# Performance work log

Hardware: AMD Instinct MI355X
Metric: run time of the kernel (lower is better)

Reference implementation:

```python
import jax, jax.numpy as jnp
import numpy as np
import math

DIM = 2048
N_HEADS = 16
N_KV_HEADS = 8
HEAD_DIM = DIM // N_HEADS  # 128
N_REP = N_HEADS // N_KV_HEADS  # 2
SEQ = 2048
BATCH = 1
HIDDEN = 5632  # round_up(int(2*(4*2048)/3), 256)
NORM_EPS = 1e-5
LN_EPS = 1e-5  # torch.nn.LayerNorm default
ROPE_THETA = 10000.0


def rmsnorm(x, w, eps=NORM_EPS):
    x32 = x.astype(jnp.float32)
    n = x32 * jax.lax.rsqrt(jnp.mean(x32 * x32, axis=-1, keepdims=True) + eps)
    return n.astype(x.dtype) * w


def layernorm(x, w, b, eps=LN_EPS):
    mu = jnp.mean(x, axis=-1, keepdims=True)
    var = jnp.mean((x - mu) ** 2, axis=-1, keepdims=True)
    return (x - mu) * jax.lax.rsqrt(var + eps) * w + b


def apply_rope(x, cos, sin):
    # x: [B,S,H,hd]; cos/sin: [S, hd//2] -> complex multiply on (even, odd) pairs
    xr = x.reshape(*x.shape[:-1], HEAD_DIM // 2, 2)
    x0, x1 = xr[..., 0], xr[..., 1]
    c = cos[None, :, None, :]
    s = sin[None, :, None, :]
    o0 = x0 * c - x1 * s
    o1 = x0 * s + x1 * c
    return jnp.stack([o0, o1], axis=-1).reshape(x.shape)


def setup_inputs() -> dict:
    key = jax.random.key(0)
    ks = jax.random.split(key, 10)
    scale = 0.02
    x = jax.random.normal(ks[0], (BATCH, SEQ, DIM), jnp.float32)
    # RoPE tables
    inv_freq = 1.0 / (ROPE_THETA ** (jnp.arange(0, HEAD_DIM, 2, dtype=jnp.float32) / HEAD_DIM))
    ang = jnp.arange(SEQ, dtype=jnp.float32)[:, None] * inv_freq[None, :]  # [S, hd//2]
    freqs_cos = jnp.cos(ang)
    freqs_sin = jnp.sin(ang)
    # causal additive mask
    mask = jnp.where(jnp.tril(jnp.ones((SEQ, SEQ), bool)), 0.0, -1e9).astype(jnp.float32)
    wqkv = jax.random.normal(ks[1], ((N_HEADS + 2 * N_KV_HEADS) * HEAD_DIM, DIM), jnp.float32) * scale
    wo = jax.random.normal(ks[2], (DIM, N_HEADS * HEAD_DIM), jnp.float32) * scale
    qn_w = jnp.ones((HEAD_DIM,), jnp.float32)
    qn_b = jnp.zeros((HEAD_DIM,), jnp.float32)
    kn_w = jnp.ones((HEAD_DIM,), jnp.float32)
    kn_b = jnp.zeros((HEAD_DIM,), jnp.float32)
    attn_norm_w = jnp.ones((DIM,), jnp.float32)
    ffn_norm_w = jnp.ones((DIM,), jnp.float32)
    w13 = jax.random.normal(ks[3], (2 * HIDDEN, DIM), jnp.float32) * scale
    w2 = jax.random.normal(ks[4], (DIM, HIDDEN), jnp.float32) * scale
    return dict(x=x, freqs_cos=freqs_cos, freqs_sin=freqs_sin, mask=mask,
                wqkv=wqkv, wo=wo, qn_w=qn_w, qn_b=qn_b, kn_w=kn_w, kn_b=kn_b,
                attn_norm_w=attn_norm_w, ffn_norm_w=ffn_norm_w, w13=w13, w2=w2)


def reference(x, freqs_cos, freqs_sin, mask, wqkv, wo, qn_w, qn_b, kn_w, kn_b,
              attn_norm_w, ffn_norm_w, w13, w2):
    B, S, _ = x.shape
    # ---- attention sublayer (pre-norm) ----
    h = rmsnorm(x, attn_norm_w)
    qkv = h @ wqkv.T  # [B,S,(H+2KV)*hd]
    q_sz = N_HEADS * HEAD_DIM
    kv_sz = N_KV_HEADS * HEAD_DIM
    q = qkv[..., :q_sz].reshape(B, S, N_HEADS, HEAD_DIM)
    k = qkv[..., q_sz:q_sz + kv_sz].reshape(B, S, N_KV_HEADS, HEAD_DIM)
    v = qkv[..., q_sz + kv_sz:].reshape(B, S, N_KV_HEADS, HEAD_DIM)
    # QK-LayerNorm (per head_dim)
    q = layernorm(q, qn_w, qn_b)
    k = layernorm(k, kn_w, kn_b)
    # RoPE
    q = apply_rope(q, freqs_cos, freqs_sin)
    k = apply_rope(k, freqs_cos, freqs_sin)
    # GQA: repeat kv heads (interleaved like torch repeat_interleave on head dim)
    k = jnp.repeat(k, N_REP, axis=2)
    v = jnp.repeat(v, N_REP, axis=2)
    # scores with fp32 softmax
    scores = jnp.einsum('bqhd,bkhd->bhqk', q, k) / math.sqrt(HEAD_DIM)
    scores = scores + mask[None, None, :, :]
    p = jax.nn.softmax(scores.astype(jnp.float32), axis=-1).astype(q.dtype)
    o = jnp.einsum('bhqk,bkhd->bqhd', p, v).reshape(B, S, N_HEADS * HEAD_DIM)
    attn_out = o @ wo.T
    h = x + attn_out
    # ---- SwiGLU FFN sublayer ----
    g = rmsnorm(h, ffn_norm_w)
    x13 = g @ w13.T
    x1, x3 = x13[..., :HIDDEN], x13[..., HIDDEN:]
    out = h + (jax.nn.silu(x1) * x3) @ w2.T
    return out
```

## Files before the change

### kernel.cpp

```cpp
#include <hip/hip_runtime.h>
#include <math.h>

#define DIM 2048
#define SEQ 2048
#define NH 16
#define NKV 8
#define HD 128
#define HIDDEN 5632
#define QKV_N 4096
#define FF_N 11264

typedef __attribute__((ext_vector_type(8))) short s16x8;
typedef __attribute__((ext_vector_type(4))) float f32x4;

#define GPTR(p) ((const __attribute__((address_space(1))) void*)(p))
#define LPTR(p) ((__attribute__((address_space(3))) void*)(p))

#define CFENCE() __asm__ __volatile__("" ::: "memory")
#define BAR() do { CFENCE(); __builtin_amdgcn_s_barrier(); CFENCE(); } while (0)

__device__ __forceinline__ unsigned short f2bf(float f) {
    union { float f; unsigned u; } v; v.f = f;
    unsigned r = v.u + 0x7fff + ((v.u >> 16) & 1);
    return (unsigned short)(r >> 16);
}
__device__ __forceinline__ float bf2f(unsigned short s) {
    union { unsigned u; float f; } v; v.u = ((unsigned)s) << 16;
    return v.f;
}

__global__ __launch_bounds__(256) void k_cvt(const float* __restrict__ src,
                                             unsigned short* __restrict__ dst, int n4) {
    int i = blockIdx.x * 256 + threadIdx.x;
    if (i < n4) {
        float4 v = ((const float4*)src)[i];
        ushort4 o;
        o.x = f2bf(v.x); o.y = f2bf(v.y); o.z = f2bf(v.z); o.w = f2bf(v.w);
        ((ushort4*)dst)[i] = o;
    }
}

__global__ __launch_bounds__(256) void k_rmsnorm(const float* __restrict__ x,
                                                 const float* __restrict__ w,
                                                 unsigned short* __restrict__ out) {
    int row = blockIdx.x;
    int tid = threadIdx.x, wv = tid >> 6, lane = tid & 63;
    const float* xr = x + (size_t)row * DIM;
    float4 a = ((const float4*)xr)[tid * 2];
    float4 b = ((const float4*)xr)[tid * 2 + 1];
    float ss = a.x*a.x + a.y*a.y + a.z*a.z + a.w*a.w
             + b.x*b.x + b.y*b.y + b.z*b.z + b.w*b.w;
    for (int off = 32; off >= 1; off >>= 1) ss += __shfl_xor(ss, off);
    __shared__ float red[4];
    if (lane == 0) red[wv] = ss;
    __syncthreads();
    float tot = red[0] + red[1] + red[2] + red[3];
    float rs = rsqrtf(tot * (1.0f / DIM) + 1e-5f);
    float4 wa = ((const float4*)w)[tid * 2];
    float4 wb = ((const float4*)w)[tid * 2 + 1];
    ushort4 o0, o1;
    o0.x = f2bf(a.x * rs * wa.x); o0.y = f2bf(a.y * rs * wa.y);
    o0.z = f2bf(a.z * rs * wa.z); o0.w = f2bf(a.w * rs * wa.w);
    o1.x = f2bf(b.x * rs * wb.x); o1.y = f2bf(b.y * rs * wb.y);
    o1.z = f2bf(b.z * rs * wb.z); o1.w = f2bf(b.w * rs * wb.w);
    ushort4* orow = (ushort4*)(out + (size_t)row * DIM);
    orow[tid * 2] = o0; orow[tid * 2 + 1] = o1;
}

template<int ID>
__global__ __launch_bounds__(512, 2) void k_gemm256(
    const unsigned short* __restrict__ A, const unsigned short* __restrict__ B,
    int M, int N, int K, int Kslice,
    float* __restrict__ Cf, unsigned short* __restrict__ Cb,
    const float* __restrict__ add, int flags) {
    __shared__ __align__(16) unsigned short As[2][16384];
    __shared__ __align__(16) unsigned short Bs[2][16384];
    int tid = threadIdx.x;
    int wv = tid >> 6, lane = tid & 63, quad = lane >> 4, l15 = lane & 15;
    int wr = wv >> 2, wc = wv & 3;
    int rowBase = blockIdx.y * 256;
    int colBase = blockIdx.x * 256;
    int kb = blockIdx.z * Kslice;
    int NT = Kslice >> 6;

    f32x4 acc[8][4] = {};

    int srow = lane >> 3;
    int schunk = lane & 7;

    auto stage = [&](const unsigned short* Mat, int matBase,
                     unsigned short (*Ls)[16384], int t, int h, int b) {
#pragma unroll
        for (int j = 0; j < 2; j++) {
            int r0 = h * 128 + (j * 8 + wv) * 8;
            int row = r0 + srow;
            int kchunk = schunk ^ (row & 7);
            const unsigned short* g = Mat + (size_t)(matBase + row) * K
                                      + (kb + t * 64 + kchunk * 8);
            __builtin_amdgcn_global_load_lds(GPTR(g), LPTR(&Ls[b][r0 * 64]), 16, 0, 0);
        }
    };
    auto LDA = [&](int b_, int mt, int ks) -> s16x8 {
        int row = wr * 128 + mt * 16 + l15;
        return *(const s16x8*)&As[b_][row * 64 + ((((ks * 4 + quad)) ^ (row & 7)) << 3)];
    };
    auto LDB = [&](int b_, int nt, int ks) -> s16x8 {
        int row = wc * 64 + nt * 16 + l15;
        return *(const s16x8*)&Bs[b_][row * 64 + ((((ks * 4 + quad)) ^ (row & 7)) << 3)];
    };

    stage(B, colBase, Bs, 0, 0, 0); stage(B, colBase, Bs, 0, 1, 0);
    stage(A, rowBase, As, 0, 0, 0); stage(A, rowBase, As, 0, 1, 0);
    if (NT > 1) {
        stage(B, colBase, Bs, 1, 0, 1); stage(B, colBase, Bs, 1, 1, 1);
        stage(A, rowBase, As, 1, 0, 1); stage(A, rowBase, As, 1, 1, 1);
        asm volatile("s_waitcnt vmcnt(8)" ::: "memory");
    } else {
        asm volatile("s_waitcnt vmcnt(0)" ::: "memory");
    }
    BAR();

    for (int T = 0; T < NT; T++) {
        const int b = T & 1;
        s16x8 a0[8], a1[8], b0[4], b1[4];
#pragma unroll
        for (int mt = 0; mt < 8; mt++) a0[mt] = LDA(b, mt, 0);
#pragma unroll
        for (int nt = 0; nt < 4; nt++) b0[nt] = LDB(b, nt, 0);
        BAR();
        asm volatile("s_waitcnt lgkmcnt(0)" ::: "memory");
        __builtin_amdgcn_s_setprio(1);
#pragma unroll
        for (int mt = 0; mt < 8; mt++) {
            acc[mt][0] = __builtin_amdgcn_mfma_f32_16x16x32_bf16(a0[mt], b0[0], acc[mt][0], 0, 0, 0);
            acc[mt][1] = __builtin_amdgcn_mfma_f32_16x16x32_bf16(a0[mt], b0[1], acc[mt][1], 0, 0, 0);
        }
        __builtin_amdgcn_s_setprio(0);
        BAR();
#pragma unroll
        for (int nt = 0; nt < 4; nt++) b1[nt] = LDB(b, nt, 1);
        BAR();
        asm volatile("s_waitcnt lgkmcnt(0)" ::: "memory");
        __builtin_amdgcn_s_setprio(1);
#pragma unroll
        for (int mt = 0; mt < 8; mt++) {
            acc[mt][2] = __builtin_amdgcn_mfma_f32_16x16x32_bf16(a0[mt], b0[2], acc[mt][2], 0, 0, 0);
            acc[mt][3] = __builtin_amdgcn_mfma_f32_16x16x32_bf16(a0[mt], b0[3], acc[mt][3], 0, 0, 0);
        }
        __builtin_amdgcn_s_setprio(0);
        BAR();
#pragma unroll
        for (int mt = 0; mt < 8; mt++) a1[mt] = LDA(b, mt, 1);
        if (T + 2 < NT) { stage(B, colBase, Bs, T + 2, 0, b); stage(B, colBase, Bs, T + 2, 1, b); }
        BAR();
        asm volatile("s_waitcnt lgkmcnt(0)" ::: "memory");
        __builtin_amdgcn_s_setprio(1);
#pragma unroll
        for (int mt = 0; mt < 8; mt++) {
            acc[mt][0] = __builtin_amdgcn_mfma_f32_16x16x32_bf16(a1[mt], b1[0], acc[mt][0], 0, 0, 0);
            acc[mt][1] = __builtin_amdgcn_mfma_f32_16x16x32_bf16(a1[mt], b1[1], acc[mt][1], 0, 0, 0);
        }
        __builtin_amdgcn_s_setprio(0);
        BAR();
        if (T + 2 < NT) { stage(A, rowBase, As, T + 2, 0, b); stage(A, rowBase, As, T + 2, 1, b); }
        BAR();
        __builtin_amdgcn_s_setprio(1);
#pragma unroll
        for (int mt = 0; mt < 8; mt++) {
            acc[mt][2] = __builtin_amdgcn_mfma_f32_16x16x32_bf16(a1[mt], b1[2], acc[mt][2], 0, 0, 0);
            acc[mt][3] = __builtin_amdgcn_mfma_f32_16x16x32_bf16(a1[mt], b1[3], acc[mt][3], 0, 0, 0);
        }
        __builtin_amdgcn_s_setprio(0);
        if (T + 2 < NT) asm volatile("s_waitcnt vmcnt(8)" ::: "memory");
        else            asm volatile("s_waitcnt vmcnt(0)" ::: "memory");
        BAR();
    }

    float* Cfz = Cf ? Cf + (size_t)blockIdx.z * M * N : nullptr;
#pragma unroll
    for (int mt = 0; mt < 8; mt++)
#pragma unroll
        for (int nt = 0; nt < 4; nt++)
#pragma unroll
            for (int r = 0; r < 4; r++) {
                int row = rowBase + wr * 128 + mt * 16 + quad * 4 + r;
                int col = colBase + wc * 64 + nt * 16 + l15;
                size_t idx = (size_t)row * N + col;
                float v = acc[mt][nt][r];
                if (flags == 1) v += add[idx];
                if (flags == 2) Cb[idx] = f2bf(v);
                else            Cfz[idx] = v;
            }
}

__global__ __launch_bounds__(256) void k_red5(const float* __restrict__ p,
                                              size_t pstride,
                                              const float* __restrict__ res,
                                              float* __restrict__ o, int n4) {
    int i = blockIdx.x * 256 + threadIdx.x;
    if (i < n4) {
        float4 r = ((const float4*)res)[i];
#pragma unroll
        for (int z = 0; z < 4; z++) {
            float4 v = ((const float4*)(p + z * pstride))[i];
            r.x += v.x; r.y += v.y; r.z += v.z; r.w += v.w;
        }
        ((float4*)o)[i] = r;
    }
}

__global__ __launch_bounds__(256) void k_qknorm_rope(
    const float* __restrict__ qkv,
    const float* __restrict__ qw, const float* __restrict__ qb,
    const float* __restrict__ kw, const float* __restrict__ kb,
    const float* __restrict__ fcos, const float* __restrict__ fsin,
    unsigned short* __restrict__ qout, unsigned short* __restrict__ kfrag) {
    int wv = threadIdx.x >> 6, lane = threadIdx.x & 63;
    int hl = blockIdx.y;
    int s = blockIdx.x * 4 + wv;
    bool isq = hl < 16;
    float2 xv = *(const float2*)&qkv[(size_t)s * QKV_N + hl * HD + 2 * lane];
    float sum = xv.x + xv.y, ssq = xv.x * xv.x + xv.y * xv.y;
    for (int off = 32; off >= 1; off >>= 1) {
        sum += __shfl_xor(sum, off);
        ssq += __shfl_xor(ssq, off);
    }
    float mu = sum * (1.0f / HD);
    float var = ssq * (1.0f / HD) - mu * mu;
    float rs = rsqrtf(var + 1e-5f);
    const float* w_ = isq ? qw : kw;
    const float* b_ = isq ? qb : kb;
    float n0 = (xv.x - mu) * rs * w_[2 * lane]     + b_[2 * lane];
    float n1 = (xv.y - mu) * rs * w_[2 * lane + 1] + b_[2 * lane + 1];
    float c = fcos[s * 64 + lane], sn = fsin[s * 64 + lane];
    float o0 = n0 * c - n1 * sn;
    float o1 = n0 * sn + n1 * c;
    if (isq) {
        const float sc = 0.12751744f;
        o0 *= sc; o1 *= sc;
        unsigned val = (unsigned)f2bf(o0) | ((unsigned)f2bf(o1) << 16);
        *(unsigned*)&qout[((size_t)hl * SEQ + s) * HD + 2 * lane] = val;
    } else {
        int kvh = hl - 16;
        int kt = s >> 6, key = s & 63;
        int dg = lane >> 2, j = (2 * lane) & 7;
        unsigned val = (unsigned)f2bf(o0) | ((unsigned)f2bf(o1) << 16);
        size_t idx = (((size_t)(kvh * 32 + kt) * 16 + dg) * 64 + key) * 8 + j;
        *(unsigned*)&kfrag[idx] = val;
    }
}

__global__ __launch_bounds__(256) void k_vprep(const float* __restrict__ qkv,
                                               unsigned short* __restrict__ vfrag) {
    __shared__ unsigned short lv[64][132];
    int kvh = blockIdx.y, kt = blockIdx.x, tid = threadIdx.x;
#pragma unroll
    for (int it = 0; it < 8; it++) {
        int li = it * 256 + tid;
        int row = li >> 5;
        int c4 = (li & 31) * 4;
        float4 v = *(const float4*)&qkv[(size_t)(kt * 64 + row) * QKV_N + 3072 + kvh * HD + c4];
        lv[row][c4] = f2bf(v.x); lv[row][c4 + 1] = f2bf(v.y);
        lv[row][c4 + 2] = f2bf(v.z); lv[row][c4 + 3] = f2bf(v.w);
    }
    __syncthreads();
    size_t base = (size_t)(kvh * 32 + kt) * 8192;
#pragma unroll
    for (int it = 0; it < 16; it++) {
        int o2 = it * 256 + tid;
        int e = o2 * 2;
        int r = e & 7, d = (e >> 3) & 127, kg = e >> 10;
        unsigned val = (unsigned)lv[kg * 8 + r][d] | ((unsigned)lv[kg * 8 + r + 1][d] << 16);
        *(unsigned*)&vfrag[base + e] = val;
    }
}

__global__ __launch_bounds__(256) void k_flash(
    const unsigned short* __restrict__ q,
    const unsigned short* __restrict__ kfrag,
    const unsigned short* __restrict__ vfrag,
    unsigned short* __restrict__ o) {
    __shared__ __align__(16) unsigned short Ks[2][8192];
    __shared__ __align__(16) unsigned short Vs[2][8192];
    __shared__ __align__(16) unsigned short Ps[4][16 * 72];
    int h = blockIdx.x & 15;
    int qt = 31 - (blockIdx.x >> 4);
    int kvh = h >> 1;
    int tid = threadIdx.x, wv = tid >> 6, lane = tid & 63, quad = lane >> 4, l15 = lane & 15;
    int qbase = qt * 64;

    s16x8 qf[4];
    {
        const unsigned short* qp = q + ((size_t)h * SEQ + qbase + wv * 16 + l15) * HD + quad * 8;
#pragma unroll
        for (int ks = 0; ks < 4; ks++) qf[ks] = *(const s16x8*)(qp + ks * 32);
    }
    f32x4 oacc[8] = {};
    float mst[4], lst[4];
#pragma unroll
    for (int r = 0; r < 4; r++) { mst[r] = -3e38f; lst[r] = 0.f; }

    auto issueKV = [&](int kt, int b) {
        size_t kb = (size_t)(kvh * 32 + kt) * 8192;
#pragma unroll
        for (int i = 0; i < 4; i++) {
            int s0 = i * 256 + wv * 64;
            __builtin_amdgcn_global_load_lds(GPTR(kfrag + kb + (size_t)(s0 + lane) * 8), LPTR(&Ks[b][s0 * 8]), 16, 0, 0);
            __builtin_amdgcn_global_load_lds(GPTR(vfrag + kb + (size_t)(s0 + lane) * 8), LPTR(&Vs[b][s0 * 8]), 16, 0, 0);
        }
    };

    issueKV(0, 0);
    for (int kt = 0; kt <= qt; kt++) {
        int b = kt & 1;
        __syncthreads();
        if (kt < qt) issueKV(kt + 1, b ^ 1);

        f32x4 sacc[4];
#pragma unroll
        for (int nt = 0; nt < 4; nt++) {
            f32x4 a = {};
#pragma unroll
            for (int ks = 0; ks < 4; ks++) {
                s16x8 kf = *(const s16x8*)&Ks[b][((ks * 4 + quad) * 64 + nt * 16 + l15) * 8];
                a = __builtin_amdgcn_mfma_f32_16x16x32_bf16(qf[ks], kf, a, 0, 0, 0);
            }
            sacc[nt] = a;
        }
        if (kt == qt) {
#pragma unroll
            for (int nt = 0; nt < 4; nt++) {
                int colg = kt * 64 + nt * 16 + l15;
#pragma unroll
                for (int r = 0; r < 4; r++) {
                    int rowg = qbase + wv * 16 + quad * 4 + r;
                    if (colg > rowg) sacc[nt][r] = -3e38f;
                }
            }
        }
        unsigned short* Pw = Ps[wv];
#pragma unroll
        for (int r = 0; r < 4; r++) {
            float mx = fmaxf(fmaxf(sacc[0][r], sacc[1][r]), fmaxf(sacc[2][r], sacc[3][r]));
#pragma unroll
            for (int off = 1; off < 16; off <<= 1) mx = fmaxf(mx, __shfl_xor(mx, off));
            float mnew = fmaxf(mst[r], mx);
            float alpha = exp2f(mst[r] - mnew);
            float psum = 0.f;
#pragma unroll
            for (int nt = 0; nt < 4; nt++) {
                float p = exp2f(sacc[nt][r] - mnew);
                psum += p;
                Pw[(quad * 4 + r) * 72 + nt * 16 + l15] = f2bf(p);
            }
#pragma unroll
            for (int off = 1; off < 16; off <<= 1) psum += __shfl_xor(psum, off);
            lst[r] = lst[r] * alpha + psum;
            mst[r] = mnew;
#pragma unroll
            for (int vt = 0; vt < 8; vt++) oacc[vt][r] *= alpha;
        }
#pragma unroll
        for (int ks = 0; ks < 2; ks++) {
            s16x8 pf = *(const s16x8*)&Pw[l15 * 72 + ks * 32 + quad * 8];
#pragma unroll
            for (int vt = 0; vt < 8; vt++) {
                s16x8 vf = *(const s16x8*)&Vs[b][((ks * 4 + quad) * 128 + vt * 16 + l15) * 8];
                oacc[vt] = __builtin_amdgcn_mfma_f32_16x16x32_bf16(pf, vf, oacc[vt], 0, 0, 0);
            }
        }
    }
#pragma unroll
    for (int r = 0; r < 4; r++) {
        float inv = 1.0f / lst[r];
        int row = qbase + wv * 16 + quad * 4 + r;
#pragma unroll
        for (int vt = 0; vt < 8; vt++)
            o[(size_t)row * DIM + h * HD + vt * 16 + l15] = f2bf(oacc[vt][r] * inv);
    }
}

__global__ __launch_bounds__(256) void k_silu(const unsigned short* __restrict__ x13,
                                              unsigned short* __restrict__ y) {
    int gid = blockIdx.x * 256 + threadIdx.x;
    int s = gid / 1408;
    int j4 = (gid - s * 1408) * 4;
    const unsigned short* p1 = x13 + (size_t)s * FF_N + j4;
    const unsigned short* p3 = p1 + HIDDEN;
    ushort4 a = *(const ushort4*)p1;
    ushort4 b = *(const ushort4*)p3;
    ushort4 o;
    {
        float x1 = bf2f(a.x), x3 = bf2f(b.x);
        o.x = f2bf(x1 / (1.f + __expf(-x1)) * x3);
    }
    {
        float x1 = bf2f(a.y), x3 = bf2f(b.y);
        o.y = f2bf(x1 / (1.f + __expf(-x1)) * x3);
    }
    {
        float x1 = bf2f(a.z), x3 = bf2f(b.z);
        o.z = f2bf(x1 / (1.f + __expf(-x1)) * x3);
    }
    {
        float x1 = bf2f(a.w), x3 = bf2f(b.w);
        o.w = f2bf(x1 / (1.f + __expf(-x1)) * x3);
    }
    *(ushort4*)&y[(size_t)s * HIDDEN + j4] = o;
}

extern "C" void kernel_launch(void* const* d_in, const int* in_sizes, int n_in,
                              void* d_out, int out_size, void* d_ws, size_t ws_size,
                              hipStream_t stream) {
    const float* x    = (const float*)d_in[0];
    const float* fcos = (const float*)d_in[1];
    const float* fsin = (const float*)d_in[2];
    const float* wqkv = (const float*)d_in[4];
    const float* wo   = (const float*)d_in[5];
    const float* qn_w = (const float*)d_in[6];
    const float* qn_b = (const float*)d_in[7];
    const float* kn_w = (const float*)d_in[8];
    const float* kn_b = (const float*)d_in[9];
    const float* anw  = (const float*)d_in[10];
    const float* fnw  = (const float*)d_in[11];
    const float* w13  = (const float*)d_in[12];
    const float* w2   = (const float*)d_in[13];
    float* out = (float*)d_out;
    char* ws = (char*)d_ws;

    size_t off = 0;
    auto alloc = [&](size_t bytes) { size_t o = off; off += (bytes + 255) & ~(size_t)255; return o; };
    unsigned short* wqkv_b = (unsigned short*)(ws + alloc((size_t)QKV_N * DIM * 2));
    unsigned short* wo_b   = (unsigned short*)(ws + alloc((size_t)DIM * DIM * 2));
    unsigned short* w13_b  = (unsigned short*)(ws + alloc((size_t)FF_N * DIM * 2));
    unsigned short* w2_b   = (unsigned short*)(ws + alloc((size_t)DIM * HIDDEN * 2));
    unsigned short* xn     = (unsigned short*)(ws + alloc((size_t)SEQ * DIM * 2));
    float*          qkv    = (float*)         (ws + alloc((size_t)SEQ * QKV_N * 4));
    unsigned short* qb_    = (unsigned short*)(ws + alloc((size_t)NH * SEQ * HD * 2));
    unsigned short* kfr    = (unsigned short*)(ws + alloc((size_t)NKV * SEQ * HD * 2));
    unsigned short* vfr    = (unsigned short*)(ws + alloc((size_t)NKV * SEQ * HD * 2));
    unsigned short* ob     = (unsigned short*)(ws + alloc((size_t)SEQ * DIM * 2));
    float*          hbuf   = (float*)         (ws + alloc((size_t)SEQ * DIM * 4));
    unsigned short* gb     = (unsigned short*)(ws + alloc((size_t)SEQ * DIM * 2));
    unsigned short* x13b   = (unsigned short*)(ws + alloc((size_t)SEQ * FF_N * 2));
    unsigned short* yb     = (unsigned short*)(ws + alloc((size_t)SEQ * HIDDEN * 2));
    float*          pp     = (float*)         (ws + alloc((size_t)4 * SEQ * DIM * 4));
    const size_t pstride = (size_t)SEQ * DIM;

    k_cvt<<<8192, 256, 0, stream>>>(wqkv, wqkv_b, QKV_N * DIM / 4);
    k_cvt<<<4096, 256, 0, stream>>>(wo, wo_b, DIM * DIM / 4);
    k_cvt<<<22528, 256, 0, stream>>>(w13, w13_b, FF_N * DIM / 4);
    k_cvt<<<11264, 256, 0, stream>>>(w2, w2_b, DIM * HIDDEN / 4);

    k_rmsnorm<<<SEQ, 256, 0, stream>>>(x, anw, xn);
    k_gemm256<0><<<dim3(QKV_N / 256, SEQ / 256), 512, 0, stream>>>(
        xn, wqkv_b, SEQ, QKV_N, DIM, DIM, qkv, nullptr, nullptr, 0);
    k_qknorm_rope<<<dim3(SEQ / 4, NH + NKV), 256, 0, stream>>>(
        qkv, qn_w, qn_b, kn_w, kn_b, fcos, fsin, qb_, kfr);
    k_vprep<<<dim3(SEQ / 64, NKV), 256, 0, stream>>>(qkv, vfr);
    k_flash<<<NH * (SEQ / 64), 256, 0, stream>>>(qb_, kfr, vfr, ob);
    k_gemm256<1><<<dim3(DIM / 256, SEQ / 256, 4), 512, 0, stream>>>(
        ob, wo_b, SEQ, DIM, DIM, DIM / 4, pp, nullptr, nullptr, 0);
    k_red5<<<SEQ * DIM / 1024, 256, 0, stream>>>(pp, pstride, x, hbuf, SEQ * DIM / 4);
    k_rmsnorm<<<SEQ, 256, 0, stream>>>(hbuf, fnw, gb);
    k_gemm256<2><<<dim3(FF_N / 256, SEQ / 256), 512, 0, stream>>>(
        gb, w13_b, SEQ, FF_N, DIM, DIM, nullptr, x13b, nullptr, 2);
    k_silu<<<SEQ * (HIDDEN / 4) / 256, 256, 0, stream>>>(x13b, yb);
    k_gemm256<3><<<dim3(DIM / 256, SEQ / 256, 4), 512, 0, stream>>>(
        yb, w2_b, SEQ, DIM, HIDDEN, HIDDEN / 4, pp, nullptr, nullptr, 0);
    k_red5<<<SEQ * DIM / 1024, 256, 0, stream>>>(pp, pstride, hbuf, out, SEQ * DIM / 4);
}
```

Before: 747.4 us.

## Split-K QKV GEMM, XCD-aware block remap, and restructured GEMM main loop

The QKV projection GEMM now uses a 2-way split-K with partial sums written to the shared partial buffer. The following q/k-norm-rope and V-prep kernels add the two partials on load, so no separate reduction pass is needed. All GEMM launches remap workgroup indices so consecutive tiles land on the same XCD, aiming for better L2 reuse. The main loop is reorganised from four barrier-separated MFMA phases into two larger phases with fewer barriers, with all global staging issued together. This trades extra fp32 partial traffic and a changed LDS-reuse/synchronisation pattern for more occupancy on the small QKV grid.

New measurement: 677.8 us. 1.1x faster.

```diff
diff --git a/kernel.cpp b/kernel.cpp
--- a/kernel.cpp
+++ b/kernel.cpp
@@ -78,9 +78,19 @@
     int tid = threadIdx.x;
     int wv = tid >> 6, lane = tid & 63, quad = lane >> 4, l15 = lane & 15;
     int wr = wv >> 2, wc = wv & 3;
-    int rowBase = blockIdx.y * 256;
-    int colBase = blockIdx.x * 256;
-    int kb = blockIdx.z * Kslice;
+
+    int gx = gridDim.x, gy = gridDim.y;
+    int n_wg = gx * gy * gridDim.z;
+    int lin = (blockIdx.z * gy + blockIdx.y) * gx + blockIdx.x;
+    int q8 = n_wg >> 3, r8 = n_wg & 7;
+    int xcd = lin & 7, idx8 = lin >> 3;
+    int nl = (xcd < r8 ? xcd * (q8 + 1) : r8 * (q8 + 1) + (xcd - r8) * q8) + idx8;
+    int bx = nl % gx; int rest = nl / gx;
+    int by = rest % gy; int bz = rest / gy;
+
+    int rowBase = by * 256;
+    int colBase = bx * 256;
+    int kb = bz * Kslice;
     int NT = Kslice >> 6;
 
     f32x4 acc[8][4] = {};
@@ -122,51 +132,36 @@
 
     for (int T = 0; T < NT; T++) {
         const int b = T & 1;
-        s16x8 a0[8], a1[8], b0[4], b1[4];
+        s16x8 a0[8], b0[4], b1[4];
+#pragma unroll
+        for (int nt = 0; nt < 4; nt++) b0[nt] = LDB(b, nt, 0);
 #pragma unroll
         for (int mt = 0; mt < 8; mt++) a0[mt] = LDA(b, mt, 0);
 #pragma unroll
-        for (int nt = 0; nt < 4; nt++) b0[nt] = LDB(b, nt, 0);
-        BAR();
-        asm volatile("s_waitcnt lgkmcnt(0)" ::: "memory");
+        for (int nt = 0; nt < 4; nt++) b1[nt] = LDB(b, nt, 1);
         __builtin_amdgcn_s_setprio(1);
 #pragma unroll
         for (int mt = 0; mt < 8; mt++) {
             acc[mt][0] = __builtin_amdgcn_mfma_f32_16x16x32_bf16(a0[mt], b0[0], acc[mt][0], 0, 0, 0);
             acc[mt][1] = __builtin_amdgcn_mfma_f32_16x16x32_bf16(a0[mt], b0[1], acc[mt][1], 0, 0, 0);
-        }
-        __builtin_amdgcn_s_setprio(0);
-        BAR();
-#pragma unroll
-        for (int nt = 0; nt < 4; nt++) b1[nt] = LDB(b, nt, 1);
-        BAR();
-        asm volatile("s_waitcnt lgkmcnt(0)" ::: "memory");
-        __builtin_amdgcn_s_setprio(1);
-#pragma unroll
-        for (int mt = 0; mt < 8; mt++) {
             acc[mt][2] = __builtin_amdgcn_mfma_f32_16x16x32_bf16(a0[mt], b0[2], acc[mt][2], 0, 0, 0);
             acc[mt][3] = __builtin_amdgcn_mfma_f32_16x16x32_bf16(a0[mt], b0[3], acc[mt][3], 0, 0, 0);
         }
         __builtin_amdgcn_s_setprio(0);
+        s16x8 a1[8];
+#pragma unroll
+        for (int mt = 0; mt < 8; mt++) a1[mt] = LDA(b, mt, 1);
+        asm volatile("s_waitcnt lgkmcnt(0)" ::: "memory");
         BAR();
-#pragma unroll
-        for (int mt = 0; mt < 8; mt++) a1[mt] = LDA(b, mt, 1);
-        if (T + 2 < NT) { stage(B, colBase, Bs, T + 2, 0, b); stage(B, colBase, Bs, T + 2, 1, b); }
-        BAR();
-        asm volatile("s_waitcnt lgkmcnt(0)" ::: "memory");
+        if (T + 2 < NT) {
+            stage(B, colBase, Bs, T + 2, 0, b); stage(B, colBase, Bs, T + 2, 1, b);
+            stage(A, rowBase, As, T + 2, 0, b); stage(A, rowBase, As, T + 2, 1, b);
+        }
         __builtin_amdgcn_s_setprio(1);
 #pragma unroll
         for (int mt = 0; mt < 8; mt++) {
             acc[mt][0] = __builtin_amdgcn_mfma_f32_16x16x32_bf16(a1[mt], b1[0], acc[mt][0], 0, 0, 0);
             acc[mt][1] = __builtin_amdgcn_mfma_f32_16x16x32_bf16(a1[mt], b1[1], acc[mt][1], 0, 0, 0);
-        }
-        __builtin_amdgcn_s_setprio(0);
-        BAR();
-        if (T + 2 < NT) { stage(A, rowBase, As, T + 2, 0, b); stage(A, rowBase, As, T + 2, 1, b); }
-        BAR();
-        __builtin_amdgcn_s_setprio(1);
-#pragma unroll
-        for (int mt = 0; mt < 8; mt++) {
             acc[mt][2] = __builtin_amdgcn_mfma_f32_16x16x32_bf16(a1[mt], b1[2], acc[mt][2], 0, 0, 0);
             acc[mt][3] = __builtin_amdgcn_mfma_f32_16x16x32_bf16(a1[mt], b1[3], acc[mt][3], 0, 0, 0);
         }
@@ -176,7 +171,7 @@
         BAR();
     }
 
-    float* Cfz = Cf ? Cf + (size_t)blockIdx.z * M * N : nullptr;
+    float* Cfz = Cf ? Cf + (size_t)bz * M * N : nullptr;
 #pragma unroll
     for (int mt = 0; mt < 8; mt++)
 #pragma unroll
@@ -210,7 +205,7 @@
 }
 
 __global__ __launch_bounds__(256) void k_qknorm_rope(
-    const float* __restrict__ qkv,
+    const float* __restrict__ qkv0, const float* __restrict__ qkv1,
     const float* __restrict__ qw, const float* __restrict__ qb,
     const float* __restrict__ kw, const float* __restrict__ kb,
     const float* __restrict__ fcos, const float* __restrict__ fsin,
@@ -219,7 +214,10 @@
     int hl = blockIdx.y;
     int s = blockIdx.x * 4 + wv;
     bool isq = hl < 16;
-    float2 xv = *(const float2*)&qkv[(size_t)s * QKV_N + hl * HD + 2 * lane];
+    size_t base = (size_t)s * QKV_N + hl * HD + 2 * lane;
+    float2 u = *(const float2*)&qkv0[base];
+    float2 w2v = *(const float2*)&qkv1[base];
+    float2 xv; xv.x = u.x + w2v.x; xv.y = u.y + w2v.y;
     float sum = xv.x + xv.y, ssq = xv.x * xv.x + xv.y * xv.y;
     for (int off = 32; off >= 1; off >>= 1) {
         sum += __shfl_xor(sum, off);
@@ -250,7 +248,8 @@
     }
 }
 
-__global__ __launch_bounds__(256) void k_vprep(const float* __restrict__ qkv,
+__global__ __launch_bounds__(256) void k_vprep(const float* __restrict__ qkv0,
+                                               const float* __restrict__ qkv1,
                                                unsigned short* __restrict__ vfrag) {
     __shared__ unsigned short lv[64][132];
     int kvh = blockIdx.y, kt = blockIdx.x, tid = threadIdx.x;
@@ -259,7 +258,10 @@
         int li = it * 256 + tid;
         int row = li >> 5;
         int c4 = (li & 31) * 4;
-        float4 v = *(const float4*)&qkv[(size_t)(kt * 64 + row) * QKV_N + 3072 + kvh * HD + c4];
+        size_t base = (size_t)(kt * 64 + row) * QKV_N + 3072 + kvh * HD + c4;
+        float4 v = *(const float4*)&qkv0[base];
+        float4 v1 = *(const float4*)&qkv1[base];
+        v.x += v1.x; v.y += v1.y; v.z += v1.z; v.w += v1.w;
         lv[row][c4] = f2bf(v.x); lv[row][c4 + 1] = f2bf(v.y);
         lv[row][c4 + 2] = f2bf(v.z); lv[row][c4 + 3] = f2bf(v.w);
     }
@@ -435,7 +437,6 @@
     unsigned short* w13_b  = (unsigned short*)(ws + alloc((size_t)FF_N * DIM * 2));
     unsigned short* w2_b   = (unsigned short*)(ws + alloc((size_t)DIM * HIDDEN * 2));
     unsigned short* xn     = (unsigned short*)(ws + alloc((size_t)SEQ * DIM * 2));
-    float*          qkv    = (float*)         (ws + alloc((size_t)SEQ * QKV_N * 4));
     unsigned short* qb_    = (unsigned short*)(ws + alloc((size_t)NH * SEQ * HD * 2));
     unsigned short* kfr    = (unsigned short*)(ws + alloc((size_t)NKV * SEQ * HD * 2));
     unsigned short* vfr    = (unsigned short*)(ws + alloc((size_t)NKV * SEQ * HD * 2));
@@ -446,6 +447,8 @@
     unsigned short* yb     = (unsigned short*)(ws + alloc((size_t)SEQ * HIDDEN * 2));
     float*          pp     = (float*)         (ws + alloc((size_t)4 * SEQ * DIM * 4));
     const size_t pstride = (size_t)SEQ * DIM;
+    float* qkvp  = pp;
+    const float* qkvp1 = qkvp + (size_t)SEQ * QKV_N;
 
     k_cvt<<<8192, 256, 0, stream>>>(wqkv, wqkv_b, QKV_N * DIM / 4);
     k_cvt<<<4096, 256, 0, stream>>>(wo, wo_b, DIM * DIM / 4);
@@ -453,11 +456,11 @@
     k_cvt<<<11264, 256, 0, stream>>>(w2, w2_b, DIM * HIDDEN / 4);
 
     k_rmsnorm<<<SEQ, 256, 0, stream>>>(x, anw, xn);
-    k_gemm256<0><<<dim3(QKV_N / 256, SEQ / 256), 512, 0, stream>>>(
-        xn, wqkv_b, SEQ, QKV_N, DIM, DIM, qkv, nullptr, nullptr, 0);
+    k_gemm256<0><<<dim3(QKV_N / 256, SEQ / 256, 2), 512, 0, stream>>>(
+        xn, wqkv_b, SEQ, QKV_N, DIM, DIM / 2, qkvp, nullptr, nullptr, 0);
     k_qknorm_rope<<<dim3(SEQ / 4, NH + NKV), 256, 0, stream>>>(
-        qkv, qn_w, qn_b, kn_w, kn_b, fcos, fsin, qb_, kfr);
-    k_vprep<<<dim3(SEQ / 64, NKV), 256, 0, stream>>>(qkv, vfr);
+        qkvp, qkvp1, qn_w, qn_b, kn_w, kn_b, fcos, fsin, qb_, kfr);
+    k_vprep<<<dim3(SEQ / 64, NKV), 256, 0, stream>>>(qkvp, qkvp1, vfr);
     k_flash<<<NH * (SEQ / 64), 256, 0, stream>>>(qb_, kfr, vfr, ob);
     k_gemm256<1><<<dim3(DIM / 256, SEQ / 256, 4), 512, 0, stream>>>(
         ob, wo_b, SEQ, DIM, DIM, DIM / 4, pp, nullptr, nullptr, 0);
```
